# Kernel tuning notes

Measured on AMD Instinct MI355X. Metric: run time of the kernel, lower is better.

## Reference

```python
import jax, jax.numpy as jnp
import numpy as np

N, E, F, CUTOFF = 50000, 500000, 64, 5.0
EPS_CN, EPS_LN = 1e-8, 1e-5


def _xavier(k, shape):
    lim = float(np.sqrt(6.0 / (shape[0] + shape[1])))
    return jax.random.uniform(k, shape, jnp.float32, -lim, lim)


def setup_inputs() -> dict:
    key = jax.random.key(0)
    ks = jax.random.split(key, 20)
    vn = jax.random.normal(ks[5], (E, 3), jnp.float32)
    vn = vn / jnp.linalg.norm(vn, axis=-1, keepdims=True)  # unit direction vectors
    return {
        "node_s": jax.random.normal(ks[0], (N, 1, F), jnp.float32),
        "node_v": jax.random.normal(ks[1], (N, 3, F), jnp.float32),
        "edge_s": jax.random.normal(ks[2], (E, 1, F), jnp.float32),
        "edge_v": jax.random.normal(ks[3], (E, 3, F), jnp.float32),
        "dist": jax.random.uniform(ks[4], (E, 1), jnp.float32) * CUTOFF,
        "vctr_norm": vn,
        "src": jax.random.randint(ks[6], (E,), 0, N),
        "dst": jax.random.randint(ks[7], (E,), 0, N),
        "W_nn": _xavier(ks[8], (2 * F, F)), "b_nn": jnp.zeros((F,), jnp.float32),
        "W_ep": _xavier(ks[9], (F, F)), "b_ep": jnp.zeros((F,), jnp.float32),
        "W_g1": _xavier(ks[10], (F, F)), "b_g1": jnp.zeros((F,), jnp.float32),
        "W_g2": _xavier(ks[11], (F, F)), "b_g2": jnp.zeros((F,), jnp.float32),
        "W_ev": _xavier(ks[12], (F, 3 * F)), "b_ev": jnp.zeros((3 * F,), jnp.float32),
        "W_nvout": _xavier(ks[13], (F, 3 * F)),
        "W_nvc": _xavier(ks[14], (2 * F, F)), "b_nvc": jnp.zeros((F,), jnp.float32),
        "W_nvp": _xavier(ks[15], (F, 2 * F)),
        "W_nsp": _xavier(ks[16], (F, 2 * F)), "b_nsp": jnp.zeros((2 * F,), jnp.float32),
        "ln_gamma": jnp.ones((F,), jnp.float32), "ln_beta": jnp.zeros((F,), jnp.float32),
        "cn_scale": jnp.ones((F,), jnp.float32),
    }


def reference(node_s, node_v, edge_s, edge_v, dist, vctr_norm, src, dst,
              W_nn, b_nn, W_ep, b_ep, W_g1, b_g1, W_g2, b_g2, W_ev, b_ev,
              W_nvout, W_nvc, b_nvc, W_nvp, W_nsp, b_nsp, ln_gamma, ln_beta, cn_scale):
    n_nodes = node_s.shape[0]
    # cosine cutoff [E,1]
    c = 0.5 * (jnp.cos(jnp.pi * dist / CUTOFF) + 1.0) * (dist < CUTOFF).astype(dist.dtype)
    # ---- edge scalar update (gather src/dst, small MLPs) ----
    nn_in = jnp.concatenate([node_s[src], node_s[dst]], axis=-1)        # [E,1,2F]
    node_neighbors = nn_in @ W_nn + b_nn                                # [E,1,F]
    edge_message = node_neighbors * (edge_s @ W_ep + b_ep)              # [E,1,F]
    h = jax.nn.silu(edge_message @ W_g1 + b_g1)                         # GateMLP hidden
    es_upd = (h @ W_g2 + b_g2) * c[..., None]                           # [E,1,F]
    # ---- edge vector update ----
    vch = es_upd @ W_ev + b_ev                                          # [E,1,3F]
    nch, ech, rch = jnp.split(vch, 3, axis=-1)
    ev_upd = node_v[src] * nch + edge_v * ech + vctr_norm[..., None] * rch  # [E,3,F]
    ev_upd = ev_upd * c[..., None]
    # ---- scatter-mean to destination nodes ----
    deg = jax.ops.segment_sum(jnp.ones((src.shape[0],), node_s.dtype), dst, num_segments=n_nodes)
    denom = jnp.maximum(deg, 1.0)[:, None, None]
    n_ev = jax.ops.segment_sum(ev_upd, dst, num_segments=n_nodes) / denom  # [N,3,F]
    n_es = jax.ops.segment_sum(es_upd, dst, num_segments=n_nodes) / denom  # [N,1,F]
    # ---- node vector update ----
    nv_o1, nv_o2, nv_o3 = jnp.split(n_ev @ W_nvout, 3, axis=-1)          # each [N,3,F]
    v_in = jnp.concatenate([n_es, jnp.linalg.norm(nv_o3, axis=1, keepdims=True)], axis=-1)  # [N,1,2F]
    v_channel = v_in @ W_nvc + b_nvc                                     # [N,1,F]
    nv_upd = nv_o1 * v_channel + nv_o2                                   # [N,3,F]
    # ---- node scalar update ----
    nvp1, nvp2 = jnp.split(nv_upd @ W_nvp, 2, axis=-1)                   # [N,3,F] each
    ns1, ns2 = jnp.split(jax.nn.silu(n_es @ W_nsp + b_nsp), 2, axis=-1)  # [N,1,F] each
    nv_dot = jnp.sum(nvp1 * nvp2, axis=1, keepdims=True)                 # [N,1,F]
    ns_upd = nv_dot * ns1 + ns2                                          # [N,1,F]
    # ---- residuals + norms ----
    node_s_out = ns_upd + node_s
    node_v_out = nv_upd + node_v
    edge_s_out = es_upd + edge_s
    edge_v_out = ev_upd + edge_v
    # CoorsNorm: normalize over the 3D axis, learnable per-channel scale
    vnorm = jnp.linalg.norm(node_v_out, axis=1, keepdims=True)
    node_v_out = node_v_out / jnp.maximum(vnorm, EPS_CN) * cn_scale
    # LayerNorm over feature dim
    mu = jnp.mean(node_s_out, axis=-1, keepdims=True)
    var = jnp.var(node_s_out, axis=-1, keepdims=True)
    node_s_out = (node_s_out - mu) / jnp.sqrt(var + EPS_LN) * ln_gamma + ln_beta
    return node_s_out, node_v_out, edge_s_out, edge_v_out
```

## Files before the change

kernel.cpp:

```cpp
#include <hip/hip_runtime.h>
#include <hip/hip_bf16.h>
#include <math.h>

typedef __attribute__((ext_vector_type(8))) short bf16x8;
typedef __attribute__((ext_vector_type(4))) float f32x4;

#define MFMA16(a, b, c) __builtin_amdgcn_mfma_f32_16x16x32_bf16((a), (b), (c), 0, 0, 0)

__device__ __forceinline__ float silu_f(float x) { return x / (1.0f + expf(-x)); }

__device__ __forceinline__ unsigned short f2bf(float f) {
  union { __hip_bfloat16 h; unsigned short u; } c;
  c.h = __float2bfloat16(f);
  return c.u;
}
__device__ __forceinline__ unsigned pk2(float a, float b) {
  return (unsigned)f2bf(a) | ((unsigned)f2bf(b) << 16);
}
__device__ __forceinline__ float bfu(unsigned short u) {
  union { unsigned u32; float f; } c;
  c.u32 = (unsigned)u << 16;
  return c.f;
}

__device__ __forceinline__ bf16x8 ld_act(const unsigned short* buf, int strideB, int ks, int lane) {
  int row = lane & 15;
  int off = row * strideB + ks * 64 + ((lane >> 4) << 4);
  off ^= (row & 7) << 4;
  return *(const bf16x8*)((const char*)buf + off);
}

__device__ __forceinline__ bf16x8 ld_w(const unsigned short* Wt, int rowbase, int strideB, int ks, int lane) {
  return *(const bf16x8*)((const char*)Wt + (size_t)(rowbase + (lane & 15)) * strideB + ks * 64 + ((lane >> 4) << 4));
}

__global__ void wprep_all(const float* __restrict__ W_nn, const float* __restrict__ W_ep,
                          const float* __restrict__ W_g1, const float* __restrict__ W_g2,
                          const float* __restrict__ W_ev,
                          unsigned short* __restrict__ wnn_t, unsigned short* __restrict__ wep_t,
                          unsigned short* __restrict__ wg1_t, unsigned short* __restrict__ wg2_t,
                          unsigned short* __restrict__ wev_t) {
  int idx = blockIdx.x * 256 + threadIdx.x;
  if (idx < 8192) {
    int n = idx >> 7, k = idx & 127;
    wnn_t[idx] = f2bf(W_nn[k * 64 + n]);
  } else if (idx < 12288) {
    int t = idx - 8192; int n = t >> 6, k = t & 63;
    wep_t[t] = f2bf(W_ep[k * 64 + n]);
  } else if (idx < 16384) {
    int t = idx - 12288; int n = t >> 6, k = t & 63;
    wg1_t[t] = f2bf(W_g1[k * 64 + n]);
  } else if (idx < 20480) {
    int t = idx - 16384; int n = t >> 6, k = t & 63;
    wg2_t[t] = f2bf(W_g2[k * 64 + n]);
  } else if (idx < 32768) {
    int t = idx - 20480; int n = t >> 6, k = t & 63;
    wev_t[t] = f2bf(W_ev[k * 192 + n]);
  }
}

__global__ void hist_kernel(const int* __restrict__ dst, int* __restrict__ cnt, int E) {
  int i = blockIdx.x * blockDim.x + threadIdx.x;
  if (i < E) atomicAdd(&cnt[dst[i]], 1);
}

__global__ __launch_bounds__(1024) void scan_kernel(int* __restrict__ cnt,
                                                    int* __restrict__ rowstart, int N) {
  __shared__ int wsum[16];
  const int tid = threadIdx.x;
  const int wv = tid >> 6;
  int carry = 0;
  for (int base = 0; base < N; base += 1024) {
    int i = base + tid;
    int v = (i < N) ? cnt[i] : 0;
    int x = v;
    #pragma unroll
    for (int o = 1; o < 64; o <<= 1) {
      int y = __shfl_up(x, o);
      if ((tid & 63) >= o) x += y;
    }
    if ((tid & 63) == 63) wsum[wv] = x;
    __syncthreads();
    if (tid < 16) {
      int s = wsum[tid];
      #pragma unroll
      for (int o = 1; o < 16; o <<= 1) {
        int y = __shfl_up(s, o);
        if (tid >= o) s += y;
      }
      wsum[tid] = s;
    }
    __syncthreads();
    int woff = (wv > 0) ? wsum[wv - 1] : 0;
    if (i < N) {
      int excl = carry + woff + x - v;
      rowstart[i] = excl;
      cnt[i] = excl;
    }
    carry += wsum[15];
    __syncthreads();
  }
  if (tid == 0) rowstart[N] = carry;
}

__global__ void scatter_kernel(const int* __restrict__ dst, int* __restrict__ cursor,
                               int* __restrict__ elist, int* __restrict__ epos, int E) {
  int i = blockIdx.x * blockDim.x + threadIdx.x;
  if (i < E) {
    int pos = atomicAdd(&cursor[dst[i]], 1);
    elist[pos] = i;
    epos[i] = pos;
  }
}

__global__ __launch_bounds__(256, 4) void edge_kernel(
    const float* __restrict__ node_s, const float* __restrict__ node_v,
    const float* __restrict__ edge_s, const float* __restrict__ edge_v,
    const float* __restrict__ dist,   const float* __restrict__ vctr,
    const int* __restrict__ src,      const int* __restrict__ dst,
    const int* __restrict__ epos,
    const unsigned short* __restrict__ wnn_t, const float* __restrict__ b_nn,
    const unsigned short* __restrict__ wep_t, const float* __restrict__ b_ep,
    const unsigned short* __restrict__ wg1_t, const float* __restrict__ b_g1,
    const unsigned short* __restrict__ wg2_t, const float* __restrict__ b_g2,
    const unsigned short* __restrict__ wev_t, const float* __restrict__ b_ev,
    float* __restrict__ es_out, float* __restrict__ ev_out,
    unsigned short* __restrict__ raw_es, unsigned short* __restrict__ raw_ev,
    int use_raw, int E, int n_tiles)
{
  __shared__ __align__(16) unsigned short lds[4 * 2048];
  const int wid  = threadIdx.x >> 6;
  const int lane = threadIdx.x & 63;
  const int tile = blockIdx.x * 4 + wid;
  if (tile >= n_tiles) return;
  const int ebase = tile * 16;
  unsigned short* bufA = lds + wid * 2048;
  const size_t Estride = (size_t)E * 64;

  const int m  = lane & 15;
  const int nb = lane >> 4;

  {
    const int sm = lane >> 5;
    const int kk = lane & 31;
    #pragma unroll
    for (int p = 0; p < 8; ++p) {
      int le = p * 2 + sm;
      int e = ebase + le; if (e >= E) e = E - 1;
      int s = src[e], d = dst[e];
      float2 vs = *(const float2*)(node_s + (size_t)s * 64 + 2 * kk);
      float2 vd = *(const float2*)(node_s + (size_t)d * 64 + 2 * kk);
      unsigned swz = (le & 7) << 4;
      *(unsigned*)((char*)bufA + ((le * 256 + kk * 4) ^ swz))       = pk2(vs.x, vs.y);
      *(unsigned*)((char*)bufA + ((le * 256 + 128 + kk * 4) ^ swz)) = pk2(vd.x, vd.y);
    }
  }
  __builtin_amdgcn_wave_barrier();

  const int e = (ebase + m < E) ? ebase + m : E - 1;
  const float dd_ = dist[e];
  const float cc = (dd_ < 5.0f) ? 0.5f * (cosf(3.14159265358979f * dd_ * 0.2f) + 1.0f) : 0.0f;
  const int s_nd = src[e];

  const f32x4 z4 = {0.0f, 0.0f, 0.0f, 0.0f};
  const unsigned swzm = (m & 7) << 4;

  const int tme  = lane >> 3;
  const int tseg = lane & 7;
  int tpos0 = -1, tpos1 = -1;
  if (use_raw) {
    if (ebase + tme < E)     tpos0 = epos[ebase + tme];
    if (ebase + 8 + tme < E) tpos1 = epos[ebase + 8 + tme];
  }

  bf16x8 a0 = ld_act(bufA, 256, 0, lane), a1 = ld_act(bufA, 256, 1, lane);
  bf16x8 a2 = ld_act(bufA, 256, 2, lane), a3 = ld_act(bufA, 256, 3, lane);

  const float* esrow = edge_s + (size_t)e * 64;
  bf16x8 b0, b1;
  {
    const int k8 = (lane >> 4) << 3;
    f32x4 p0 = *(const f32x4*)(esrow + k8);
    f32x4 p1 = *(const f32x4*)(esrow + k8 + 4);
    f32x4 q0 = *(const f32x4*)(esrow + 32 + k8);
    f32x4 q1 = *(const f32x4*)(esrow + 32 + k8 + 4);
    union { bf16x8 v; uint4 u; } cb;
    cb.u.x = pk2(p0.x, p0.y); cb.u.y = pk2(p0.z, p0.w);
    cb.u.z = pk2(p1.x, p1.y); cb.u.w = pk2(p1.z, p1.w);
    b0 = cb.v;
    cb.u.x = pk2(q0.x, q0.y); cb.u.y = pk2(q0.z, q0.w);
    cb.u.z = pk2(q1.x, q1.y); cb.u.w = pk2(q1.z, q1.w);
    b1 = cb.v;
  }
  __builtin_amdgcn_wave_barrier();

  #pragma unroll
  for (int nt = 0; nt < 4; ++nt) {
    f32x4 aN = z4, aP = z4;
    aN = MFMA16(ld_w(wnn_t, nt * 16, 256, 0, lane), a0, aN);
    aN = MFMA16(ld_w(wnn_t, nt * 16, 256, 1, lane), a1, aN);
    aN = MFMA16(ld_w(wnn_t, nt * 16, 256, 2, lane), a2, aN);
    aN = MFMA16(ld_w(wnn_t, nt * 16, 256, 3, lane), a3, aN);
    aP = MFMA16(ld_w(wep_t, nt * 16, 128, 0, lane), b0, aP);
    aP = MFMA16(ld_w(wep_t, nt * 16, 128, 1, lane), b1, aP);
    f32x4 bn = *(const f32x4*)(b_nn + nt * 16 + nb * 4);
    f32x4 bp = *(const f32x4*)(b_ep + nt * 16 + nb * 4);
    float e0 = (aN.x + bn.x) * (aP.x + bp.x);
    float e1 = (aN.y + bn.y) * (aP.y + bp.y);
    float e2 = (aN.z + bn.z) * (aP.z + bp.z);
    float e3 = (aN.w + bn.w) * (aP.w + bp.w);
    uint2 w2; w2.x = pk2(e0, e1); w2.y = pk2(e2, e3);
    *(uint2*)((char*)bufA + ((m * 128 + nt * 32 + nb * 8) ^ swzm)) = w2;
  }
  __builtin_amdgcn_wave_barrier();

  bf16x8 c0 = ld_act(bufA, 128, 0, lane), c1 = ld_act(bufA, 128, 1, lane);
  __builtin_amdgcn_wave_barrier();
  #pragma unroll
  for (int nt = 0; nt < 4; ++nt) {
    f32x4 aH = z4;
    aH = MFMA16(ld_w(wg1_t, nt * 16, 128, 0, lane), c0, aH);
    aH = MFMA16(ld_w(wg1_t, nt * 16, 128, 1, lane), c1, aH);
    f32x4 bg = *(const f32x4*)(b_g1 + nt * 16 + nb * 4);
    uint2 w2;
    w2.x = pk2(silu_f(aH.x + bg.x), silu_f(aH.y + bg.y));
    w2.y = pk2(silu_f(aH.z + bg.z), silu_f(aH.w + bg.w));
    *(uint2*)((char*)bufA + ((m * 128 + nt * 32 + nb * 8) ^ swzm)) = w2;
  }
  __builtin_amdgcn_wave_barrier();

  bf16x8 d0 = ld_act(bufA, 128, 0, lane), d1 = ld_act(bufA, 128, 1, lane);
  __builtin_amdgcn_wave_barrier();
  float* eorow = es_out + (size_t)e * 64;
  #pragma unroll
  for (int nt = 0; nt < 4; ++nt) {
    f32x4 aS = z4;
    aS = MFMA16(ld_w(wg2_t, nt * 16, 128, 0, lane), d0, aS);
    aS = MFMA16(ld_w(wg2_t, nt * 16, 128, 1, lane), d1, aS);
    f32x4 bg = *(const f32x4*)(b_g2 + nt * 16 + nb * 4);
    float u0 = (aS.x + bg.x) * cc, u1 = (aS.y + bg.y) * cc;
    float u2 = (aS.z + bg.z) * cc, u3 = (aS.w + bg.w) * cc;
    const int n0 = nt * 16 + nb * 4;
    uint2 w2; w2.x = pk2(u0, u1); w2.y = pk2(u2, u3);
    *(uint2*)((char*)bufA + ((m * 128 + nt * 32 + nb * 8) ^ swzm)) = w2;
    if (ebase + m < E) {
      f32x4 r = *(const f32x4*)(esrow + n0);
      f32x4 o; o.x = u0 + r.x; o.y = u1 + r.y; o.z = u2 + r.z; o.w = u3 + r.w;
      __builtin_nontemporal_store(o, (f32x4*)(eorow + n0));
    }
  }
  __builtin_amdgcn_wave_barrier();

  bf16x8 g0 = ld_act(bufA, 128, 0, lane), g1f = ld_act(bufA, 128, 1, lane);
  if (use_raw) {
    if (tpos0 >= 0) {
      bf16x8 row = *(const bf16x8*)((const char*)bufA + ((tme * 128 + tseg * 16) ^ ((tme & 7) << 4)));
      *(bf16x8*)(raw_es + (size_t)tpos0 * 64 + tseg * 8) = row;
    }
    if (tpos1 >= 0) {
      bf16x8 row = *(const bf16x8*)((const char*)bufA + (((8 + tme) * 128 + tseg * 16) ^ (((8 + tme) & 7) << 4)));
      *(bf16x8*)(raw_es + (size_t)tpos1 * 64 + tseg * 8) = row;
    }
  }

  f32x4 accV[12];
  #pragma unroll
  for (int ch = 0; ch < 3; ++ch)
    #pragma unroll
    for (int nt = 0; nt < 4; ++nt) {
      f32x4 a = z4;
      a = MFMA16(ld_w(wev_t, ch * 64 + nt * 16, 128, 0, lane), g0,  a);
      a = MFMA16(ld_w(wev_t, ch * 64 + nt * 16, 128, 1, lane), g1f, a);
      f32x4 bv = *(const f32x4*)(b_ev + ch * 64 + nt * 16 + nb * 4);
      a.x += bv.x; a.y += bv.y; a.z += bv.z; a.w += bv.w;
      accV[ch * 4 + nt] = a;
    }

  const float* nvb = node_v + (size_t)s_nd * 192;
  const float* evb = edge_v + (size_t)e * 192;
  float* eob = ev_out + (size_t)e * 192;
  const float vnn[3] = {vctr[e * 3], vctr[e * 3 + 1], vctr[e * 3 + 2]};
  const bool live = (ebase + m < E);
  #pragma unroll
  for (int dd = 0; dd < 3; ++dd) {
    __builtin_amdgcn_wave_barrier();
    #pragma unroll
    for (int nt = 0; nt < 4; ++nt) {
      const int n0 = nt * 16 + nb * 4;
      f32x4 nv = *(const f32x4*)(nvb + dd * 64 + n0);
      f32x4 ev = __builtin_nontemporal_load((const f32x4*)(evb + dd * 64 + n0));
      float eu0 = (nv.x * accV[nt].x + ev.x * accV[4 + nt].x + vnn[dd] * accV[8 + nt].x) * cc;
      float eu1 = (nv.y * accV[nt].y + ev.y * accV[4 + nt].y + vnn[dd] * accV[8 + nt].y) * cc;
      float eu2 = (nv.z * accV[nt].z + ev.z * accV[4 + nt].z + vnn[dd] * accV[8 + nt].z) * cc;
      float eu3 = (nv.w * accV[nt].w + ev.w * accV[4 + nt].w + vnn[dd] * accV[8 + nt].w) * cc;
      if (live) {
        f32x4 o; o.x = eu0 + ev.x; o.y = eu1 + ev.y; o.z = eu2 + ev.z; o.w = eu3 + ev.w;
        __builtin_nontemporal_store(o, (f32x4*)(eob + dd * 64 + n0));
      }
      uint2 w2; w2.x = pk2(eu0, eu1); w2.y = pk2(eu2, eu3);
      *(uint2*)((char*)bufA + ((m * 128 + nt * 32 + nb * 8) ^ swzm)) = w2;
    }
    __builtin_amdgcn_wave_barrier();
    if (use_raw) {
      unsigned short* plane = raw_ev + (size_t)dd * Estride;
      if (tpos0 >= 0) {
        bf16x8 row = *(const bf16x8*)((const char*)bufA + ((tme * 128 + tseg * 16) ^ ((tme & 7) << 4)));
        *(bf16x8*)(plane + (size_t)tpos0 * 64 + tseg * 8) = row;
      }
      if (tpos1 >= 0) {
        bf16x8 row = *(const bf16x8*)((const char*)bufA + (((8 + tme) * 128 + tseg * 16) ^ (((8 + tme) & 7) << 4)));
        *(bf16x8*)(plane + (size_t)tpos1 * 64 + tseg * 8) = row;
      }
    }
  }
}

__device__ __forceinline__ void ld4(const float* p, float o[4]) {
  f32x4 v = *(const f32x4*)p;
  o[0] = v.x; o[1] = v.y; o[2] = v.z; o[3] = v.w;
}

__global__ __launch_bounds__(256) void node_kernel(
    const float* __restrict__ node_s, const float* __restrict__ node_v,
    const float* __restrict__ edge_s, const float* __restrict__ edge_v,
    const float* __restrict__ es_r,   const float* __restrict__ ev_r,
    const unsigned short* __restrict__ raw_es, const unsigned short* __restrict__ raw_ev,
    const int* __restrict__ rowstart, const int* __restrict__ elist, int use_raw,
    const float* __restrict__ W_nvout,
    const float* __restrict__ W_nvc, const float* __restrict__ b_nvc,
    const float* __restrict__ W_nvp,
    const float* __restrict__ W_nsp, const float* __restrict__ b_nsp,
    const float* __restrict__ ln_g, const float* __restrict__ ln_b,
    const float* __restrict__ cn_s,
    float* __restrict__ ns_out, float* __restrict__ nv_out, int N, int E)
{
  __shared__ __align__(16) float scm[4 * 8 * 68];
  const int wid = threadIdx.x >> 6, lane = threadIdx.x & 63;
  const int n = blockIdx.x * 4 + wid;
  if (n >= N) return;
  float* S = &scm[wid * 8 * 68];

  const int rs = rowstart[n], re = rowstart[n + 1];
  float nes = 0.0f, nev0 = 0.0f, nev1 = 0.0f, nev2 = 0.0f;
  if (use_raw) {
    const size_t Estride = (size_t)E * 64;
    const unsigned short* pe = raw_es + (size_t)rs * 64 + lane;
    const unsigned short* v0 = raw_ev + (size_t)rs * 64 + lane;
    const unsigned short* v1 = v0 + Estride;
    const unsigned short* v2 = v1 + Estride;
    const int cntE = re - rs;
    int i = 0;
    for (; i + 1 < cntE; i += 2) {
      unsigned short e0 = pe[i * 64],  e1 = pe[i * 64 + 64];
      unsigned short a0 = v0[i * 64],  a1 = v0[i * 64 + 64];
      unsigned short b0 = v1[i * 64],  b1 = v1[i * 64 + 64];
      unsigned short c0 = v2[i * 64],  c1 = v2[i * 64 + 64];
      nes  += bfu(e0) + bfu(e1);
      nev0 += bfu(a0) + bfu(a1);
      nev1 += bfu(b0) + bfu(b1);
      nev2 += bfu(c0) + bfu(c1);
    }
    if (i < cntE) {
      nes  += bfu(pe[i * 64]);
      nev0 += bfu(v0[i * 64]); nev1 += bfu(v1[i * 64]); nev2 += bfu(v2[i * 64]);
    }
  } else {
    for (int idx = rs; idx < re; ++idx) {
      int e = elist[idx];
      size_t b64 = (size_t)e * 64, b192 = (size_t)e * 192;
      nes  += es_r[b64 + lane]        - edge_s[b64 + lane];
      nev0 += ev_r[b192 + lane]       - edge_v[b192 + lane];
      nev1 += ev_r[b192 + 64 + lane]  - edge_v[b192 + 64 + lane];
      nev2 += ev_r[b192 + 128 + lane] - edge_v[b192 + 128 + lane];
    }
  }
  const float inv = 1.0f / fmaxf((float)(re - rs), 1.0f);
  nes *= inv; nev0 *= inv; nev1 *= inv; nev2 *= inv;

  S[0 * 68 + lane] = nev0; S[1 * 68 + lane] = nev1;
  S[2 * 68 + lane] = nev2; S[3 * 68 + lane] = nes;
  __builtin_amdgcn_wave_barrier();

  float o1[3] = {}, o2[3] = {}, o3[3] = {};
  for (int k = 0; k < 64; k += 4) {
    float a0[4], a1[4], a2[4];
    ld4(S + 0 * 68 + k, a0); ld4(S + 1 * 68 + k, a1); ld4(S + 2 * 68 + k, a2);
    #pragma unroll
    for (int kk = 0; kk < 4; ++kk) {
      float w0 = W_nvout[(k + kk) * 192 + lane];
      float w1 = W_nvout[(k + kk) * 192 + 64 + lane];
      float w2 = W_nvout[(k + kk) * 192 + 128 + lane];
      o1[0] = fmaf(a0[kk], w0, o1[0]); o1[1] = fmaf(a1[kk], w0, o1[1]); o1[2] = fmaf(a2[kk], w0, o1[2]);
      o2[0] = fmaf(a0[kk], w1, o2[0]); o2[1] = fmaf(a1[kk], w1, o2[1]); o2[2] = fmaf(a2[kk], w1, o2[2]);
      o3[0] = fmaf(a0[kk], w2, o3[0]); o3[1] = fmaf(a1[kk], w2, o3[1]); o3[2] = fmaf(a2[kk], w2, o3[2]);
    }
  }
  float nrm = sqrtf(o3[0] * o3[0] + o3[1] * o3[1] + o3[2] * o3[2]);
  S[4 * 68 + lane] = nrm;
  __builtin_amdgcn_wave_barrier();

  float vch = 0.0f;
  for (int k = 0; k < 64; k += 4) {
    float a[4], b[4];
    ld4(S + 3 * 68 + k, a); ld4(S + 4 * 68 + k, b);
    #pragma unroll
    for (int kk = 0; kk < 4; ++kk) {
      vch = fmaf(a[kk], W_nvc[(k + kk) * 64 + lane], vch);
      vch = fmaf(b[kk], W_nvc[(64 + k + kk) * 64 + lane], vch);
    }
  }
  vch += b_nvc[lane];

  float nvu[3];
  #pragma unroll
  for (int dd = 0; dd < 3; ++dd) {
    nvu[dd] = o1[dd] * vch + o2[dd];
    S[(5 + dd) * 68 + lane] = nvu[dd];
  }
  __builtin_amdgcn_wave_barrier();

  float p1[3] = {}, p2[3] = {};
  for (int k = 0; k < 64; k += 4) {
    float a0[4], a1[4], a2[4];
    ld4(S + 5 * 68 + k, a0); ld4(S + 6 * 68 + k, a1); ld4(S + 7 * 68 + k, a2);
    #pragma unroll
    for (int kk = 0; kk < 4; ++kk) {
      float w1 = W_nvp[(k + kk) * 128 + lane];
      float w2 = W_nvp[(k + kk) * 128 + 64 + lane];
      p1[0] = fmaf(a0[kk], w1, p1[0]); p1[1] = fmaf(a1[kk], w1, p1[1]); p1[2] = fmaf(a2[kk], w1, p1[2]);
      p2[0] = fmaf(a0[kk], w2, p2[0]); p2[1] = fmaf(a1[kk], w2, p2[1]); p2[2] = fmaf(a2[kk], w2, p2[2]);
    }
  }

  float s1a = 0.0f, s2a = 0.0f;
  for (int k = 0; k < 64; k += 4) {
    float a[4];
    ld4(S + 3 * 68 + k, a);
    #pragma unroll
    for (int kk = 0; kk < 4; ++kk) {
      s1a = fmaf(a[kk], W_nsp[(k + kk) * 128 + lane], s1a);
      s2a = fmaf(a[kk], W_nsp[(k + kk) * 128 + 64 + lane], s2a);
    }
  }
  float s1 = silu_f(s1a + b_nsp[lane]);
  float s2 = silu_f(s2a + b_nsp[64 + lane]);

  float nvdot = p1[0] * p2[0] + p1[1] * p2[1] + p1[2] * p2[2];
  float nsu = nvdot * s1 + s2;

  float xs = nsu + node_s[n * 64 + lane];
  float sum = xs, sumsq = xs * xs;
  #pragma unroll
  for (int o = 32; o; o >>= 1) {
    sum += __shfl_xor(sum, o);
    sumsq += __shfl_xor(sumsq, o);
  }
  float mu = sum * (1.0f / 64.0f);
  float var = sumsq * (1.0f / 64.0f) - mu * mu;
  ns_out[n * 64 + lane] = (xs - mu) * rsqrtf(var + 1e-5f) * ln_g[lane] + ln_b[lane];

  float vv[3];
  #pragma unroll
  for (int dd = 0; dd < 3; ++dd) vv[dd] = nvu[dd] + node_v[n * 192 + dd * 64 + lane];
  float vn2 = sqrtf(vv[0] * vv[0] + vv[1] * vv[1] + vv[2] * vv[2]);
  float scale = cn_s[lane] / fmaxf(vn2, 1e-8f);
  #pragma unroll
  for (int dd = 0; dd < 3; ++dd)
    nv_out[n * 192 + dd * 64 + lane] = vv[dd] * scale;
}

extern "C" void kernel_launch(void* const* d_in, const int* in_sizes, int n_in,
                              void* d_out, int out_size, void* d_ws, size_t ws_size,
                              hipStream_t stream) {
  const float* node_s = (const float*)d_in[0];
  const float* node_v = (const float*)d_in[1];
  const float* edge_s = (const float*)d_in[2];
  const float* edge_v = (const float*)d_in[3];
  const float* dist   = (const float*)d_in[4];
  const float* vctr   = (const float*)d_in[5];
  const int*   src    = (const int*)d_in[6];
  const int*   dst    = (const int*)d_in[7];
  const float* W_nn = (const float*)d_in[8];  const float* b_nn = (const float*)d_in[9];
  const float* W_ep = (const float*)d_in[10]; const float* b_ep = (const float*)d_in[11];
  const float* W_g1 = (const float*)d_in[12]; const float* b_g1 = (const float*)d_in[13];
  const float* W_g2 = (const float*)d_in[14]; const float* b_g2 = (const float*)d_in[15];
  const float* W_ev = (const float*)d_in[16]; const float* b_ev = (const float*)d_in[17];
  const float* W_nvout = (const float*)d_in[18];
  const float* W_nvc = (const float*)d_in[19]; const float* b_nvc = (const float*)d_in[20];
  const float* W_nvp = (const float*)d_in[21];
  const float* W_nsp = (const float*)d_in[22]; const float* b_nsp = (const float*)d_in[23];
  const float* ln_g = (const float*)d_in[24]; const float* ln_b = (const float*)d_in[25];
  const float* cn_s = (const float*)d_in[26];

  const int N = in_sizes[0] / 64;
  const int E = in_sizes[2] / 64;

  float* out    = (float*)d_out;
  float* ns_out = out;
  float* nv_out = out + (size_t)N * 64;
  float* es_out = out + (size_t)N * 256;
  float* ev_out = out + (size_t)N * 256 + (size_t)E * 64;

  int* cnt      = (int*)d_ws;
  int* rowstart = cnt + N;
  int* epos     = rowstart + N + 1;
  int* elist    = epos + E;
  unsigned short* wnn_t = (unsigned short*)(elist + E);
  unsigned short* wep_t = wnn_t + 64 * 128;
  unsigned short* wg1_t = wep_t + 64 * 64;
  unsigned short* wg2_t = wg1_t + 64 * 64;
  unsigned short* wev_t = wg2_t + 64 * 64;
  size_t wend = (size_t)((char*)(wev_t + 192 * 64) - (char*)d_ws);
  size_t rawofs = (wend + 255) & ~(size_t)255;
  unsigned short* raw_es = (unsigned short*)((char*)d_ws + rawofs);
  unsigned short* raw_ev = raw_es + (size_t)E * 64;
  size_t need = rawofs + (size_t)E * 256 * sizeof(unsigned short);
  int use_raw = (ws_size >= need) ? 1 : 0;

  hipMemsetAsync(cnt, 0, (size_t)N * sizeof(int), stream);
  hist_kernel<<<(E + 255) / 256, 256, 0, stream>>>(dst, cnt, E);
  scan_kernel<<<1, 1024, 0, stream>>>(cnt, rowstart, N);
  scatter_kernel<<<(E + 255) / 256, 256, 0, stream>>>(dst, cnt, elist, epos, E);

  wprep_all<<<128, 256, 0, stream>>>(W_nn, W_ep, W_g1, W_g2, W_ev,
                                     wnn_t, wep_t, wg1_t, wg2_t, wev_t);

  int n_tiles = (E + 15) / 16;
  edge_kernel<<<(n_tiles + 3) / 4, 256, 0, stream>>>(
      node_s, node_v, edge_s, edge_v, dist, vctr, src, dst, epos,
      wnn_t, b_nn, wep_t, b_ep, wg1_t, b_g1, wg2_t, b_g2, wev_t, b_ev,
      es_out, ev_out, raw_es, raw_ev, use_raw, E, n_tiles);

  node_kernel<<<(N + 3) / 4, 256, 0, stream>>>(
      node_s, node_v, edge_s, edge_v, es_out, ev_out, raw_es, raw_ev,
      rowstart, elist, use_raw,
      W_nvout, W_nvc, b_nvc, W_nvp, W_nsp, b_nsp,
      ln_g, ln_b, cn_s, ns_out, nv_out, N, E);
}
```

Before: 993.7 us.

## Parallelize CSR scan, recompute edge-vector MFMAs per dim, raise edge occupancy

```diff
diff --git a/kernel.cpp b/kernel.cpp
--- a/kernel.cpp
+++ b/kernel.cpp
@@ -64,43 +64,60 @@
   if (i < E) atomicAdd(&cnt[dst[i]], 1);
 }
 
-__global__ __launch_bounds__(1024) void scan_kernel(int* __restrict__ cnt,
-                                                    int* __restrict__ rowstart, int N) {
+__global__ __launch_bounds__(1024) void scan1_kernel(const int* __restrict__ cnt,
+                                                     int* __restrict__ rowstart,
+                                                     int* __restrict__ bsum, int N) {
   __shared__ int wsum[16];
   const int tid = threadIdx.x;
   const int wv = tid >> 6;
-  int carry = 0;
-  for (int base = 0; base < N; base += 1024) {
-    int i = base + tid;
-    int v = (i < N) ? cnt[i] : 0;
-    int x = v;
-    #pragma unroll
-    for (int o = 1; o < 64; o <<= 1) {
-      int y = __shfl_up(x, o);
-      if ((tid & 63) >= o) x += y;
-    }
-    if ((tid & 63) == 63) wsum[wv] = x;
-    __syncthreads();
-    if (tid < 16) {
-      int s = wsum[tid];
-      #pragma unroll
-      for (int o = 1; o < 16; o <<= 1) {
-        int y = __shfl_up(s, o);
-        if (tid >= o) s += y;
-      }
-      wsum[tid] = s;
-    }
-    __syncthreads();
-    int woff = (wv > 0) ? wsum[wv - 1] : 0;
-    if (i < N) {
-      int excl = carry + woff + x - v;
-      rowstart[i] = excl;
-      cnt[i] = excl;
-    }
-    carry += wsum[15];
-    __syncthreads();
-  }
-  if (tid == 0) rowstart[N] = carry;
+  const int i = blockIdx.x * 1024 + tid;
+  int v = (i < N) ? cnt[i] : 0;
+  int x = v;
+  #pragma unroll
+  for (int o = 1; o < 64; o <<= 1) {
+    int y = __shfl_up(x, o);
+    if ((tid & 63) >= o) x += y;
+  }
+  if ((tid & 63) == 63) wsum[wv] = x;
+  __syncthreads();
+  if (tid < 16) {
+    int s = wsum[tid];
+    #pragma unroll
+    for (int o = 1; o < 16; o <<= 1) {
+      int y = __shfl_up(s, o);
+      if (tid >= o) s += y;
+    }
+    wsum[tid] = s;
+  }
+  __syncthreads();
+  int woff = (wv > 0) ? wsum[wv - 1] : 0;
+  if (i < N) rowstart[i] = woff + x - v;
+  if (tid == 0) bsum[blockIdx.x] = wsum[15];
+}
+
+__global__ void scan2_kernel(int* __restrict__ bsum, int nb) {
+  const int tid = threadIdx.x;
+  int v = (tid < nb) ? bsum[tid] : 0;
+  int x = v;
+  #pragma unroll
+  for (int o = 1; o < 64; o <<= 1) {
+    int y = __shfl_up(x, o);
+    if (tid >= o) x += y;
+  }
+  if (tid < nb) bsum[tid] = x - v;
+}
+
+__global__ __launch_bounds__(1024) void scan3_kernel(int* __restrict__ rowstart,
+                                                     int* __restrict__ cursor,
+                                                     const int* __restrict__ bsum,
+                                                     int N, int E) {
+  const int i = blockIdx.x * 1024 + threadIdx.x;
+  if (i < N) {
+    int r = rowstart[i] + bsum[blockIdx.x];
+    rowstart[i] = r;
+    cursor[i] = r;
+  }
+  if (i == 0) rowstart[N] = E;
 }
 
 __global__ void scatter_kernel(const int* __restrict__ dst, int* __restrict__ cursor,
@@ -113,7 +130,7 @@
   }
 }
 
-__global__ __launch_bounds__(256, 4) void edge_kernel(
+__global__ __launch_bounds__(256, 8) void edge_kernel(
     const float* __restrict__ node_s, const float* __restrict__ node_v,
     const float* __restrict__ edge_s, const float* __restrict__ edge_v,
     const float* __restrict__ dist,   const float* __restrict__ vctr,
@@ -255,26 +272,13 @@
   if (use_raw) {
     if (tpos0 >= 0) {
       bf16x8 row = *(const bf16x8*)((const char*)bufA + ((tme * 128 + tseg * 16) ^ ((tme & 7) << 4)));
-      *(bf16x8*)(raw_es + (size_t)tpos0 * 64 + tseg * 8) = row;
+      __builtin_nontemporal_store(row, (bf16x8*)(raw_es + (size_t)tpos0 * 64 + tseg * 8));
     }
     if (tpos1 >= 0) {
       bf16x8 row = *(const bf16x8*)((const char*)bufA + (((8 + tme) * 128 + tseg * 16) ^ (((8 + tme) & 7) << 4)));
-      *(bf16x8*)(raw_es + (size_t)tpos1 * 64 + tseg * 8) = row;
-    }
-  }
-
-  f32x4 accV[12];
-  #pragma unroll
-  for (int ch = 0; ch < 3; ++ch)
-    #pragma unroll
-    for (int nt = 0; nt < 4; ++nt) {
-      f32x4 a = z4;
-      a = MFMA16(ld_w(wev_t, ch * 64 + nt * 16, 128, 0, lane), g0,  a);
-      a = MFMA16(ld_w(wev_t, ch * 64 + nt * 16, 128, 1, lane), g1f, a);
-      f32x4 bv = *(const f32x4*)(b_ev + ch * 64 + nt * 16 + nb * 4);
-      a.x += bv.x; a.y += bv.y; a.z += bv.z; a.w += bv.w;
-      accV[ch * 4 + nt] = a;
-    }
+      __builtin_nontemporal_store(row, (bf16x8*)(raw_es + (size_t)tpos1 * 64 + tseg * 8));
+    }
+  }
 
   const float* nvb = node_v + (size_t)s_nd * 192;
   const float* evb = edge_v + (size_t)e * 192;
@@ -286,13 +290,23 @@
     __builtin_amdgcn_wave_barrier();
     #pragma unroll
     for (int nt = 0; nt < 4; ++nt) {
+      f32x4 aN = z4, aE = z4, aR = z4;
+      aN = MFMA16(ld_w(wev_t,        nt * 16, 128, 0, lane), g0,  aN);
+      aN = MFMA16(ld_w(wev_t,        nt * 16, 128, 1, lane), g1f, aN);
+      aE = MFMA16(ld_w(wev_t,  64 + nt * 16, 128, 0, lane), g0,  aE);
+      aE = MFMA16(ld_w(wev_t,  64 + nt * 16, 128, 1, lane), g1f, aE);
+      aR = MFMA16(ld_w(wev_t, 128 + nt * 16, 128, 0, lane), g0,  aR);
+      aR = MFMA16(ld_w(wev_t, 128 + nt * 16, 128, 1, lane), g1f, aR);
       const int n0 = nt * 16 + nb * 4;
+      f32x4 bv0 = *(const f32x4*)(b_ev + n0);
+      f32x4 bv1 = *(const f32x4*)(b_ev + 64 + n0);
+      f32x4 bv2 = *(const f32x4*)(b_ev + 128 + n0);
       f32x4 nv = *(const f32x4*)(nvb + dd * 64 + n0);
       f32x4 ev = __builtin_nontemporal_load((const f32x4*)(evb + dd * 64 + n0));
-      float eu0 = (nv.x * accV[nt].x + ev.x * accV[4 + nt].x + vnn[dd] * accV[8 + nt].x) * cc;
-      float eu1 = (nv.y * accV[nt].y + ev.y * accV[4 + nt].y + vnn[dd] * accV[8 + nt].y) * cc;
-      float eu2 = (nv.z * accV[nt].z + ev.z * accV[4 + nt].z + vnn[dd] * accV[8 + nt].z) * cc;
-      float eu3 = (nv.w * accV[nt].w + ev.w * accV[4 + nt].w + vnn[dd] * accV[8 + nt].w) * cc;
+      float eu0 = (nv.x * (aN.x + bv0.x) + ev.x * (aE.x + bv1.x) + vnn[dd] * (aR.x + bv2.x)) * cc;
+      float eu1 = (nv.y * (aN.y + bv0.y) + ev.y * (aE.y + bv1.y) + vnn[dd] * (aR.y + bv2.y)) * cc;
+      float eu2 = (nv.z * (aN.z + bv0.z) + ev.z * (aE.z + bv1.z) + vnn[dd] * (aR.z + bv2.z)) * cc;
+      float eu3 = (nv.w * (aN.w + bv0.w) + ev.w * (aE.w + bv1.w) + vnn[dd] * (aR.w + bv2.w)) * cc;
       if (live) {
         f32x4 o; o.x = eu0 + ev.x; o.y = eu1 + ev.y; o.z = eu2 + ev.z; o.w = eu3 + ev.w;
         __builtin_nontemporal_store(o, (f32x4*)(eob + dd * 64 + n0));
@@ -305,11 +319,11 @@
       unsigned short* plane = raw_ev + (size_t)dd * Estride;
       if (tpos0 >= 0) {
         bf16x8 row = *(const bf16x8*)((const char*)bufA + ((tme * 128 + tseg * 16) ^ ((tme & 7) << 4)));
-        *(bf16x8*)(plane + (size_t)tpos0 * 64 + tseg * 8) = row;
+        __builtin_nontemporal_store(row, (bf16x8*)(plane + (size_t)tpos0 * 64 + tseg * 8));
       }
       if (tpos1 >= 0) {
         bf16x8 row = *(const bf16x8*)((const char*)bufA + (((8 + tme) * 128 + tseg * 16) ^ (((8 + tme) & 7) << 4)));
-        *(bf16x8*)(plane + (size_t)tpos1 * 64 + tseg * 8) = row;
+        __builtin_nontemporal_store(row, (bf16x8*)(plane + (size_t)tpos1 * 64 + tseg * 8));
       }
     }
   }
@@ -505,7 +519,8 @@
   int* rowstart = cnt + N;
   int* epos     = rowstart + N + 1;
   int* elist    = epos + E;
-  unsigned short* wnn_t = (unsigned short*)(elist + E);
+  int* bsum     = elist + E;
+  unsigned short* wnn_t = (unsigned short*)(bsum + 64);
   unsigned short* wep_t = wnn_t + 64 * 128;
   unsigned short* wg1_t = wep_t + 64 * 64;
   unsigned short* wg2_t = wg1_t + 64 * 64;
@@ -517,9 +532,13 @@
   size_t need = rawofs + (size_t)E * 256 * sizeof(unsigned short);
   int use_raw = (ws_size >= need) ? 1 : 0;
 
+  const int nscan = (N + 1023) / 1024;
+
   hipMemsetAsync(cnt, 0, (size_t)N * sizeof(int), stream);
   hist_kernel<<<(E + 255) / 256, 256, 0, stream>>>(dst, cnt, E);
-  scan_kernel<<<1, 1024, 0, stream>>>(cnt, rowstart, N);
+  scan1_kernel<<<nscan, 1024, 0, stream>>>(cnt, rowstart, bsum, N);
+  scan2_kernel<<<1, 64, 0, stream>>>(bsum, nscan);
+  scan3_kernel<<<nscan, 1024, 0, stream>>>(rowstart, cnt, bsum, N, E);
   scatter_kernel<<<(E + 255) / 256, 256, 0, stream>>>(dst, cnt, elist, epos, E);
 
   wprep_all<<<128, 256, 0, stream>>>(W_nn, W_ep, W_g1, W_g2, W_ev,
```

Result: slower. 1.586 ms (+59.6%).
